# Optimization experiments

Hardware: AMD Instinct MI355X
Metric: run time of the kernel (lower is better)

Reference implementation:

```python
import jax, jax.numpy as jnp
import numpy as np


def _ln(x, g, b):
    mu = x.mean(-1, keepdims=True)
    var = ((x - mu) ** 2).mean(-1, keepdims=True)
    return (x - mu) * jax.lax.rsqrt(var + 1e-5) * g + b


def _gelu(x):
    return jax.nn.gelu(x, approximate=False)  # torch nn.GELU default (exact)


def setup_inputs() -> dict:
    key = jax.random.key(0)
    ks = iter(jax.random.split(key, 64))
    N, E, D, H, P, DT, FF, L = 30000, 480000, 128, 4, 5, 32, 512, 2
    w = lambda *s: 0.02 * jax.random.normal(next(ks), s, jnp.float32)
    return dict(
        triplet_h=jax.random.normal(next(ks), (N, D), jnp.float32),
        path_len_emb=w(P + 1, D), vp_emb=w(D), sl_emb=w(D),
        dW1=w(D, D), db1=jnp.zeros(D), dW2=w(D, H), db2=jnp.zeros(H),
        tWin=w(P, D, DT), tbin=jnp.zeros((P, DT)), tWout=w(P, DT, DT), tbout=jnp.zeros((P, DT)),
        pW1=w(DT, DT), pb1=jnp.zeros(DT), pW2=w(DT, H), pb2=jnp.zeros(H),
        ln1_g=jnp.ones((L, D)), ln1_b=jnp.zeros((L, D)),
        qkv_W=w(L, D, 3 * D), qkv_b=jnp.zeros((L, 3 * D)),
        res_ln_g=jnp.ones((L, D)), res_ln_b=jnp.zeros((L, D)),
        res_W=w(L, D, D), res_b=jnp.zeros((L, D)),
        ffn_Win=w(L, D, FF), ffn_bin=jnp.zeros((L, FF)),
        ffn_Wout=w(L, FF, D), ffn_bout=jnp.zeros((L, D)),
        src=jax.random.randint(next(ks), (E,), 0, N, jnp.int32),
        dst=jax.random.randint(next(ks), (E,), 0, N, jnp.int32),
        path=jax.random.randint(next(ks), (E, P), 0, N, jnp.int32),
        vp=jax.random.randint(next(ks), (E,), 0, 2, jnp.int32),
        sl=jax.random.randint(next(ks), (E,), 0, 2, jnp.int32),
    )


def reference(triplet_h, path_len_emb, vp_emb, sl_emb,
              dW1, db1, dW2, db2, tWin, tbin, tWout, tbout,
              pW1, pb1, pW2, pb2, ln1_g, ln1_b, qkv_W, qkv_b,
              res_ln_g, res_ln_b, res_W, res_b,
              ffn_Win, ffn_bin, ffn_Wout, ffn_bout,
              src, dst, path, vp, sl):
    N, D = triplet_h.shape
    H = dW2.shape[1]
    dh = D // H
    L = qkv_W.shape[0]
    P = path.shape[1]
    DT = tWout.shape[-1]
    scale = D ** (-0.5)

    # _featurize_path: path length embedding + virtual/self-loop overrides
    path = jnp.where(path < -99, -1, path)
    mask = path >= 0
    plen = mask.sum(-1)
    pf = path_len_emb[plen]                                   # [E, D]
    pf = jnp.where((vp == 1)[:, None], vp_emb[None, :], pf)
    pf = jnp.where((sl == 1)[:, None], sl_emb[None, :], pf)
    dist_attn = _gelu(pf @ dW1 + db1) @ dW2 + db2             # [E, H]

    # _init_path: per-position MLP on triplets, gather along paths, mean
    acc = jnp.zeros((path.shape[0], DT), triplet_h.dtype)
    for i in range(P):
        tab = _gelu(triplet_h @ tWin[i] + tbin[i]) @ tWout[i] + tbout[i]  # [N, DT]
        tab = jnp.concatenate([tab, jnp.zeros((1, DT), tab.dtype)], axis=0)
        idx = jnp.where(path[:, i] < 0, N, path[:, i])
        acc = acc + tab[idx]
    path_size = jnp.maximum(mask.sum(-1, keepdims=True), 1).astype(acc.dtype)
    path_h = acc / path_size                                  # [E, DT]
    path_attn = _gelu(path_h @ pW1 + pb1) @ pW2 + pb2         # [E, H]

    for l in range(L):
        h = _ln(triplet_h, ln1_g[l], ln1_b[l])
        qkv = (h @ qkv_W[l] + qkv_b[l]).reshape(N, 3, H, dh)
        q = qkv[:, 0] * scale
        k = qkv[:, 1]
        v = qkv[:, 2]
        # u_dot_v('Q','K'): Q lives on src, K on dst
        node_attn = jnp.einsum('ehd,ehd->eh', q[src], k[dst])  # [E, H]
        a = node_attn + dist_attn + path_attn
        # edge_softmax over incoming edges of each dst node
        m = jax.ops.segment_max(a, dst, num_segments=N)
        ex = jnp.exp(a - m[dst])
        s = jax.ops.segment_sum(ex, dst, num_segments=N)
        sa = ex / s[dst]                                       # [E, H]
        # message = src value weighted by attn, scatter-sum to dst
        he = (v[src] * sa[..., None]).reshape(-1, D)
        agg = jax.ops.segment_sum(he, dst, num_segments=N)     # [N, D]
        # Residual block
        x = triplet_h + agg @ res_W[l] + res_b[l]
        y = _ln(x, res_ln_g[l], res_ln_b[l])
        y = _gelu(y @ ffn_Win[l] + ffn_bin[l]) @ ffn_Wout[l] + ffn_bout[l]
        triplet_h = x + y
    return triplet_h
```

## Files before the change

kernel.cpp:

```cpp
#include <hip/hip_runtime.h>
#include <math.h>

#define D   128
#define H   4
#define PP  5
#define DT  32
#define FF  512
#define NL  2
#define SCALE 0.08838834764831845f

typedef _Float16 f16x8 __attribute__((ext_vector_type(8)));
typedef _Float16 f16x2 __attribute__((ext_vector_type(2)));
typedef float    f32x4 __attribute__((ext_vector_type(4)));

__device__ __forceinline__ float gelu(float x) {
    return 0.5f * x * (1.0f + erff(x * 0.7071067811865476f));
}

__device__ __forceinline__ f16x8 f16x8_zero() {
    f16x8 v;
#pragma unroll
    for (int j = 0; j < 8; ++j) v[j] = (_Float16)0.0f;
    return v;
}

#define NWP 18
struct WPrep {
    const float* src[NWP];
    _Float16*    dst[NWP];
    int K[NWP], C[NWP];
};

__global__ __launch_bounds__(256) void k_wprep(WPrep p) {
    int m = blockIdx.y;
    int n = blockIdx.x * 256 + threadIdx.x;
    int K = p.K[m], C = p.C[m];
    if (n >= K * C) return;
    int c = n / K, k = n - c * K;
    p.dst[m][n] = (_Float16)p.src[m][(size_t)k * C + c];
}

__global__ __launch_bounds__(256) void k_dist_tab(
    const float* __restrict__ ple, const float* __restrict__ vpe, const float* __restrict__ sle,
    const float* __restrict__ dW1, const float* __restrict__ db1,
    const float* __restrict__ dW2, const float* __restrict__ db2,
    float* __restrict__ dist_tab)
{
    __shared__ float pf[8][D];
    __shared__ float hid[8][D];
    int t = threadIdx.x;
    for (int i = t; i < 8 * D; i += 256) {
        int r = i >> 7, c = i & 127;
        float v;
        if (r < 6)      v = ple[r * D + c];
        else if (r == 6) v = vpe[c];
        else             v = sle[c];
        pf[r][c] = v;
    }
    __syncthreads();
    for (int i = t; i < 8 * D; i += 256) {
        int r = i >> 7, c = i & 127;
        float s = db1[c];
        for (int k = 0; k < D; ++k) s += pf[r][k] * dW1[k * D + c];
        hid[r][c] = gelu(s);
    }
    __syncthreads();
    if (t < 8 * H) {
        int r = t >> 2, h = t & 3;
        float s = db2[h];
        for (int k = 0; k < D; ++k) s += hid[r][k] * dW2[k * H + h];
        dist_tab[r * H + h] = s;
    }
}

__global__ __launch_bounds__(256) void k_tab_mfma(
    const float* __restrict__ X,
    const _Float16* __restrict__ Wt1,
    const float* __restrict__ tbin,
    const _Float16* __restrict__ Wt2,
    const float* __restrict__ tbout,
    float* __restrict__ tab, int N)
{
    __shared__ _Float16 Ah[64][136];
    __shared__ _Float16 hidS[4][16][40];
    int t = threadIdx.x;
    int n0 = blockIdx.x * 64;
#pragma unroll
    for (int i = 0; i < 4; ++i) {
        int flat = t + i * 256;
        int r = flat >> 4, c = flat & 15;
        f16x8 v = f16x8_zero();
        if (n0 + r < N) {
            const float* xp = X + (size_t)(n0 + r) * D + c * 8;
            float4 x0 = *(const float4*)xp;
            float4 x1 = *(const float4*)(xp + 4);
            v[0] = (_Float16)x0.x; v[1] = (_Float16)x0.y;
            v[2] = (_Float16)x0.z; v[3] = (_Float16)x0.w;
            v[4] = (_Float16)x1.x; v[5] = (_Float16)x1.y;
            v[6] = (_Float16)x1.z; v[7] = (_Float16)x1.w;
        }
        *(f16x8*)&Ah[r][c * 8] = v;
    }
    __syncthreads();
    int w = t >> 6, lane = t & 63;
    int rt0 = w * 16, lr = lane & 15, lg = lane >> 4;
    f16x8 a1[4];
#pragma unroll
    for (int kk = 0; kk < 4; ++kk)
        a1[kk] = *(const f16x8*)&Ah[rt0 + lr][kk * 32 + lg * 8];

    for (int i = 0; i < PP; ++i) {
#pragma unroll
        for (int ct = 0; ct < 2; ++ct) {
            int col = ct * 16 + lr;
            f32x4 c1 = {0.f, 0.f, 0.f, 0.f};
#pragma unroll
            for (int kk = 0; kk < 4; ++kk) {
                f16x8 b = *(const f16x8*)&Wt1[((size_t)i * DT + col) * 128 + kk * 32 + lg * 8];
                c1 = __builtin_amdgcn_mfma_f32_16x16x32_f16(a1[kk], b, c1, 0, 0, 0);
            }
            float bb = tbin[i * DT + col];
#pragma unroll
            for (int j = 0; j < 4; ++j)
                hidS[w][lg * 4 + j][col] = (_Float16)gelu(c1[j] + bb);
        }
        f16x8 a2 = *(const f16x8*)&hidS[w][lr][lg * 8];
#pragma unroll
        for (int ct = 0; ct < 2; ++ct) {
            int col = ct * 16 + lr;
            f32x4 c2 = {0.f, 0.f, 0.f, 0.f};
            f16x8 b2 = *(const f16x8*)&Wt2[((size_t)i * DT + col) * DT + lg * 8];
            c2 = __builtin_amdgcn_mfma_f32_16x16x32_f16(a2, b2, c2, 0, 0, 0);
            float bb = tbout[i * DT + col];
#pragma unroll
            for (int j = 0; j < 4; ++j) {
                int row = n0 + rt0 + lg * 4 + j;
                if (row < N) tab[((size_t)i * N + row) * DT + col] = c2[j] + bb;
            }
        }
    }
}

__global__ __launch_bounds__(256) void k_edge_pre(
    const int* __restrict__ path, const int* __restrict__ vp, const int* __restrict__ sl,
    const float* __restrict__ tab, const float* __restrict__ dist_tab,
    const float* __restrict__ pW1, const float* __restrict__ pb1,
    const float* __restrict__ pW2, const float* __restrict__ pb2,
    float* __restrict__ base_attn, int E, int N)
{
    __shared__ float W1t[DT][DT];
    __shared__ float W2s[DT][H];
    __shared__ float b1s[DT];
    __shared__ float b2s[H];
    __shared__ float dts[8][H];
    int t = threadIdx.x;
    for (int i = t; i < DT * DT; i += 256) {
        int k = i >> 5, c = i & 31;
        W1t[c][k] = pW1[i];
    }
    if (t < DT * H) W2s[t >> 2][t & 3] = pW2[t];
    if (t < DT) b1s[t] = pb1[t];
    if (t < H)  b2s[t] = pb2[t];
    if (t < 32) dts[t >> 2][t & 3] = dist_tab[t];
    __syncthreads();
    int e = blockIdx.x * 256 + t;
    if (e >= E) return;
    int pl = 0;
    float acc[DT];
#pragma unroll
    for (int c = 0; c < DT; ++c) acc[c] = 0.0f;
#pragma unroll
    for (int i = 0; i < PP; ++i) {
        int p = path[(size_t)e * PP + i];
        if (p < -99) p = -1;
        if (p >= 0) {
            ++pl;
            const float* row = tab + ((size_t)i * N + p) * DT;
#pragma unroll
            for (int c4 = 0; c4 < 8; ++c4) {
                float4 v = *(const float4*)(row + c4 * 4);
                acc[c4 * 4 + 0] += v.x; acc[c4 * 4 + 1] += v.y;
                acc[c4 * 4 + 2] += v.z; acc[c4 * 4 + 3] += v.w;
            }
        }
    }
    float inv = 1.0f / (float)(pl > 0 ? pl : 1);
#pragma unroll
    for (int c = 0; c < DT; ++c) acc[c] *= inv;
    float o0 = b2s[0], o1 = b2s[1], o2 = b2s[2], o3 = b2s[3];
    for (int c = 0; c < DT; ++c) {
        float s = b1s[c];
#pragma unroll
        for (int k4 = 0; k4 < 8; ++k4) {
            float4 w = *(const float4*)&W1t[c][k4 * 4];
            s += acc[k4 * 4 + 0] * w.x + acc[k4 * 4 + 1] * w.y +
                 acc[k4 * 4 + 2] * w.z + acc[k4 * 4 + 3] * w.w;
        }
        float hv = gelu(s);
        o0 += hv * W2s[c][0]; o1 += hv * W2s[c][1];
        o2 += hv * W2s[c][2]; o3 += hv * W2s[c][3];
    }
    int se = (sl[e] == 1) ? 7 : ((vp[e] == 1) ? 6 : pl);
    float4 ov = make_float4(o0 + dts[se][0], o1 + dts[se][1],
                            o2 + dts[se][2], o3 + dts[se][3]);
    *(float4*)(base_attn + (size_t)e * 4) = ov;
}

__global__ void k_count(const int* __restrict__ dst, int* __restrict__ deg, int E) {
    int e = blockIdx.x * 256 + threadIdx.x;
    if (e < E) atomicAdd(&deg[dst[e]], 1);
}

__global__ __launch_bounds__(1024) void k_scan(const int* __restrict__ deg,
                                               int* __restrict__ rowstart, int N) {
    __shared__ int sdata[1024];
    __shared__ int soff;
    int t = threadIdx.x;
    if (t == 0) soff = 0;
    for (int base = 0; base < N; base += 1024) {
        int v = (base + t < N) ? deg[base + t] : 0;
        __syncthreads();
        sdata[t] = v;
        __syncthreads();
        for (int off = 1; off < 1024; off <<= 1) {
            int x = (t >= off) ? sdata[t - off] : 0;
            __syncthreads();
            sdata[t] += x;
            __syncthreads();
        }
        int incl  = sdata[t];
        int total = sdata[1023];
        if (base + t < N) rowstart[base + t] = soff + incl - v;
        __syncthreads();
        if (t == 0) soff += total;
    }
    __syncthreads();
    if (t == 0) rowstart[N] = soff;
}

__global__ void k_scatter(const int* __restrict__ dst, const int* __restrict__ rowstart,
                          int* __restrict__ cursor, int* __restrict__ el, int E) {
    int e = blockIdx.x * 256 + threadIdx.x;
    if (e >= E) return;
    int d = dst[e];
    int pos = atomicAdd(&cursor[d], 1);
    el[rowstart[d] + pos] = e;
}

__global__ __launch_bounds__(256) void k_ln(const float* __restrict__ X, const float* __restrict__ g,
                                            const float* __restrict__ b, _Float16* __restrict__ out, int N) {
    int gw   = (blockIdx.x * 256 + threadIdx.x) >> 6;
    int lane = threadIdx.x & 63;
    if (gw >= N) return;
    const float* x = X + (size_t)gw * D;
    float a0 = x[lane], a1 = x[lane + 64];
    float s = a0 + a1;
#pragma unroll
    for (int m = 1; m < 64; m <<= 1) s += __shfl_xor(s, m);
    float mu = s * (1.0f / 128.0f);
    float d0 = a0 - mu, d1 = a1 - mu;
    float v = d0 * d0 + d1 * d1;
#pragma unroll
    for (int m = 1; m < 64; m <<= 1) v += __shfl_xor(v, m);
    float r = rsqrtf(v * (1.0f / 128.0f) + 1e-5f);
    _Float16* o = out + (size_t)gw * D;
    o[lane]      = (_Float16)(d0 * r * g[lane]      + b[lane]);
    o[lane + 64] = (_Float16)(d1 * r * g[lane + 64] + b[lane + 64]);
}


__global__ __launch_bounds__(256) void k_qkv_mfma(
    const _Float16* __restrict__ Hin, const _Float16* __restrict__ Wt,
    const float* __restrict__ bias, _Float16* __restrict__ C, int N)
{
    __shared__ _Float16 Ah[64][136];
    int t = threadIdx.x;
    int n0 = blockIdx.x * 64;
#pragma unroll
    for (int i = 0; i < 4; ++i) {
        int flat = t + i * 256;
        int r = flat >> 4, c = flat & 15;
        f16x8 v = f16x8_zero();
        if (n0 + r < N) v = *(const f16x8*)&Hin[(size_t)(n0 + r) * D + c * 8];
        *(f16x8*)&Ah[r][c * 8] = v;
    }
    __syncthreads();
    int w = t >> 6, lane = t & 63;
    int rt0 = w * 16, lr = lane & 15, lg = lane >> 4;
    f16x8 a1[4];
#pragma unroll
    for (int kk = 0; kk < 4; ++kk)
        a1[kk] = *(const f16x8*)&Ah[rt0 + lr][kk * 32 + lg * 8];
#pragma unroll 4
    for (int ct = 0; ct < 24; ++ct) {
        int col = ct * 16 + lr;
        f32x4 acc = {0.f, 0.f, 0.f, 0.f};
#pragma unroll
        for (int kk = 0; kk < 4; ++kk) {
            f16x8 b = *(const f16x8*)&Wt[(size_t)col * 128 + kk * 32 + lg * 8];
            acc = __builtin_amdgcn_mfma_f32_16x16x32_f16(a1[kk], b, acc, 0, 0, 0);
        }
        float bb = bias[col];
#pragma unroll
        for (int i = 0; i < 4; ++i) {
            int row = n0 + rt0 + lg * 4 + i;
            if (row < N) C[(size_t)row * 384 + col] = (_Float16)(acc[i] + bb);
        }
    }
}

__global__ __launch_bounds__(256) void k_res_mfma(
    const _Float16* __restrict__ Agg, const _Float16* __restrict__ Wt,
    const float* __restrict__ bias, const float* __restrict__ resid,
    float* __restrict__ Out, int N)
{
    __shared__ _Float16 Ah[64][136];
    int t = threadIdx.x;
    int n0 = blockIdx.x * 64;
#pragma unroll
    for (int i = 0; i < 4; ++i) {
        int flat = t + i * 256;
        int r = flat >> 4, c = flat & 15;
        f16x8 v = f16x8_zero();
        if (n0 + r < N) v = *(const f16x8*)&Agg[(size_t)(n0 + r) * D + c * 8];
        *(f16x8*)&Ah[r][c * 8] = v;
    }
    __syncthreads();
    int w = t >> 6, lane = t & 63;
    int rt0 = w * 16, lr = lane & 15, lg = lane >> 4;
    f16x8 a1[4];
#pragma unroll
    for (int kk = 0; kk < 4; ++kk)
        a1[kk] = *(const f16x8*)&Ah[rt0 + lr][kk * 32 + lg * 8];
#pragma unroll
    for (int ct = 0; ct < 8; ++ct) {
        int col = ct * 16 + lr;
        f32x4 acc = {0.f, 0.f, 0.f, 0.f};
#pragma unroll
        for (int kk = 0; kk < 4; ++kk) {
            f16x8 b = *(const f16x8*)&Wt[(size_t)col * 128 + kk * 32 + lg * 8];
            acc = __builtin_amdgcn_mfma_f32_16x16x32_f16(a1[kk], b, acc, 0, 0, 0);
        }
        float bb = bias[col];
#pragma unroll
        for (int i = 0; i < 4; ++i) {
            int row = n0 + rt0 + lg * 4 + i;
            if (row < N) {
                size_t o = (size_t)row * D + col;
                Out[o] = resid[o] + acc[i] + bb;
            }
        }
    }
}

__global__ __launch_bounds__(256) void k_ffn_mfma(
    const _Float16* __restrict__ Hin, const float* __restrict__ Xres,
    const _Float16* __restrict__ Wt1,
    const float* __restrict__ bin,
    const _Float16* __restrict__ Wt2,
    const float* __restrict__ bout,
    float* __restrict__ Out, int N)
{
    __shared__ _Float16 Ah[64][136];
    __shared__ _Float16 hid[64][264];
    int t = threadIdx.x;
    int n0 = blockIdx.x * 64;
#pragma unroll
    for (int i = 0; i < 4; ++i) {
        int flat = t + i * 256;
        int r = flat >> 4, c = flat & 15;
        f16x8 v = f16x8_zero();
        if (n0 + r < N) v = *(const f16x8*)&Hin[(size_t)(n0 + r) * D + c * 8];
        *(f16x8*)&Ah[r][c * 8] = v;
    }
    __syncthreads();
    int w = t >> 6, lane = t & 63;
    int rt0 = w * 16, lr = lane & 15, lg = lane >> 4;
    f16x8 a1[4];
#pragma unroll
    for (int kk = 0; kk < 4; ++kk)
        a1[kk] = *(const f16x8*)&Ah[rt0 + lr][kk * 32 + lg * 8];

    f32x4 acc2[8];
#pragma unroll
    for (int i = 0; i < 8; ++i) acc2[i] = (f32x4){0.f, 0.f, 0.f, 0.f};

    for (int ch = 0; ch < 2; ++ch) {
#pragma unroll 4
        for (int ct = 0; ct < 16; ++ct) {
            int hc = ch * 256 + ct * 16 + lr;
            f32x4 c1 = {0.f, 0.f, 0.f, 0.f};
#pragma unroll
            for (int kk = 0; kk < 4; ++kk) {
                f16x8 b = *(const f16x8*)&Wt1[(size_t)hc * 128 + kk * 32 + lg * 8];
                c1 = __builtin_amdgcn_mfma_f32_16x16x32_f16(a1[kk], b, c1, 0, 0, 0);
            }
            float bb = bin[hc];
#pragma unroll
            for (int i = 0; i < 4; ++i) {
                float v = gelu(c1[i] + bb);
                hid[rt0 + lg * 4 + i][ct * 16 + lr] = (_Float16)v;
            }
        }
#pragma unroll 2
        for (int kk2 = 0; kk2 < 8; ++kk2) {
            f16x8 a2 = *(const f16x8*)&hid[rt0 + lr][kk2 * 32 + lg * 8];
            int gk = ch * 256 + kk2 * 32 + lg * 8;
#pragma unroll
            for (int ct2 = 0; ct2 < 8; ++ct2) {
                f16x8 b2 = *(const f16x8*)&Wt2[(size_t)(ct2 * 16 + lr) * 512 + gk];
                acc2[ct2] = __builtin_amdgcn_mfma_f32_16x16x32_f16(a2, b2, acc2[ct2], 0, 0, 0);
            }
        }
    }
#pragma unroll
    for (int ct2 = 0; ct2 < 8; ++ct2) {
        int col = ct2 * 16 + lr;
        float bb = bout[col];
#pragma unroll
        for (int i = 0; i < 4; ++i) {
            int row = n0 + rt0 + lg * 4 + i;
            if (row < N) {
                size_t o = (size_t)row * D + col;
                Out[o] = Xres[o] + acc2[ct2][i] + bb;
            }
        }
    }
}

__global__ __launch_bounds__(256) void k_attn_agg(
    const _Float16* __restrict__ qkv,
    const int* __restrict__ rowstart, const int* __restrict__ el,
    const int* __restrict__ src, const float* __restrict__ base_attn,
    _Float16* __restrict__ agg, int N)
{
    int gw   = (blockIdx.x * 256 + threadIdx.x) >> 6;
    int lane = threadIdx.x & 63;
    if (gw >= N) return;
    int head = lane >> 4;
    f16x2 kk = *(const f16x2*)&qkv[(size_t)gw * 384 + 128 + 2 * lane];
    float k0 = (float)kk[0], k1 = (float)kk[1];
    int beg = rowstart[gw], end = rowstart[gw + 1];
    float s = 0.0f, a0 = 0.0f, a1 = 0.0f;
    int i = beg;
    for (; i + 4 <= end; i += 4) {
        int   e[4], sr[4];
        f16x2 qq[4], vv[4];
        float bb[4], tt[4];
#pragma unroll
        for (int j = 0; j < 4; ++j) e[j] = el[i + j];
#pragma unroll
        for (int j = 0; j < 4; ++j) sr[j] = src[e[j]];
#pragma unroll
        for (int j = 0; j < 4; ++j) {
            const _Float16* row = qkv + (size_t)sr[j] * 384;
            qq[j] = *(const f16x2*)&row[2 * lane];
            vv[j] = *(const f16x2*)&row[256 + 2 * lane];
            bb[j] = base_attn[(size_t)e[j] * 4 + head];
        }
#pragma unroll
        for (int j = 0; j < 4; ++j)
            tt[j] = (float)qq[j][0] * k0 + (float)qq[j][1] * k1;
#pragma unroll
        for (int m = 1; m <= 8; m <<= 1) {
#pragma unroll
            for (int j = 0; j < 4; ++j) tt[j] += __shfl_xor(tt[j], m);
        }
#pragma unroll
        for (int j = 0; j < 4; ++j) {
            float ex = expf(tt[j] * SCALE + bb[j]);
            s  += ex;
            a0 += ex * (float)vv[j][0];
            a1 += ex * (float)vv[j][1];
        }
    }
    for (; i < end; ++i) {
        int e  = el[i];
        int sr = src[e];
        const _Float16* row = qkv + (size_t)sr * 384;
        f16x2 qq = *(const f16x2*)&row[2 * lane];
        float t = (float)qq[0] * k0 + (float)qq[1] * k1;
#pragma unroll
        for (int m = 1; m <= 8; m <<= 1) t += __shfl_xor(t, m);
        float ex = expf(t * SCALE + base_attn[(size_t)e * 4 + head]);
        f16x2 vv = *(const f16x2*)&row[256 + 2 * lane];
        s  += ex;
        a0 += ex * (float)vv[0];
        a1 += ex * (float)vv[1];
    }
    float inv = (s > 0.0f) ? 1.0f / s : 0.0f;
    f16x2 o;
    o[0] = (_Float16)(a0 * inv);
    o[1] = (_Float16)(a1 * inv);
    *(f16x2*)&agg[(size_t)gw * D + 2 * lane] = o;
}

extern "C" void kernel_launch(void* const* d_in, const int* in_sizes, int n_in,
                              void* d_out, int out_size, void* d_ws, size_t ws_size,
                              hipStream_t stream) {
    const float* triplet_h = (const float*)d_in[0];
    const float* ple    = (const float*)d_in[1];
    const float* vpe    = (const float*)d_in[2];
    const float* sle    = (const float*)d_in[3];
    const float* dW1    = (const float*)d_in[4];
    const float* db1    = (const float*)d_in[5];
    const float* dW2    = (const float*)d_in[6];
    const float* db2    = (const float*)d_in[7];
    const float* tWin   = (const float*)d_in[8];
    const float* tbin   = (const float*)d_in[9];
    const float* tWout  = (const float*)d_in[10];
    const float* tbout  = (const float*)d_in[11];
    const float* pW1    = (const float*)d_in[12];
    const float* pb1    = (const float*)d_in[13];
    const float* pW2    = (const float*)d_in[14];
    const float* pb2    = (const float*)d_in[15];
    const float* ln1_g  = (const float*)d_in[16];
    const float* ln1_b  = (const float*)d_in[17];
    const float* qkv_W  = (const float*)d_in[18];
    const float* qkv_b  = (const float*)d_in[19];
    const float* rln_g  = (const float*)d_in[20];
    const float* rln_b  = (const float*)d_in[21];
    const float* res_W  = (const float*)d_in[22];
    const float* res_b  = (const float*)d_in[23];
    const float* fWin   = (const float*)d_in[24];
    const float* fbin   = (const float*)d_in[25];
    const float* fWout  = (const float*)d_in[26];
    const float* fbout  = (const float*)d_in[27];
    const int*   srcp   = (const int*)d_in[28];
    const int*   dstp   = (const int*)d_in[29];
    const int*   path   = (const int*)d_in[30];
    const int*   vp     = (const int*)d_in[31];
    const int*   sl     = (const int*)d_in[32];

    const int N = in_sizes[0] / D;
    const int E = in_sizes[28];

    char* ws = (char*)d_ws;
    size_t off = 0;
    auto alloc = [&](size_t bytes) -> void* {
        void* p = ws + off;
        off += (bytes + 255) & ~(size_t)255;
        return p;
    };
    float*     tab      = (float*)alloc((size_t)PP * N * DT * 4);
    float*     dist_tab = (float*)alloc(8 * H * 4);
    float*     base_attn= (float*)alloc((size_t)E * H * 4);
    int*       deg      = (int*)alloc((size_t)N * 4);
    int*       rowstart = (int*)alloc((size_t)(N + 1) * 4);
    int*       cursor   = (int*)alloc((size_t)N * 4);
    int*       el       = (int*)alloc((size_t)E * 4);
    _Float16*  hbuf     = (_Float16*)alloc((size_t)N * D * 2);
    _Float16*  qkvbuf   = (_Float16*)alloc((size_t)N * 384 * 2);
    _Float16*  aggbuf   = (_Float16*)alloc((size_t)N * D * 2);
    float*     bufA     = (float*)alloc((size_t)N * D * 4);
    float*     bufB     = (float*)alloc((size_t)N * D * 4);
    _Float16*  WtQ      = (_Float16*)alloc((size_t)NL * 384 * 128 * 2);
    _Float16*  WtR      = (_Float16*)alloc((size_t)NL * 128 * 128 * 2);
    _Float16*  Wt1      = (_Float16*)alloc((size_t)NL * 512 * 128 * 2);
    _Float16*  Wt2      = (_Float16*)alloc((size_t)NL * 128 * 512 * 2);
    _Float16*  WtTin    = (_Float16*)alloc((size_t)PP * DT * 128 * 2);
    _Float16*  WtTout   = (_Float16*)alloc((size_t)PP * DT * DT * 2);
    if (off > ws_size) return;

    hipMemsetAsync(deg,    0, (size_t)N * 4, stream);
    hipMemsetAsync(cursor, 0, (size_t)N * 4, stream);

    WPrep wp;
    wp.src[0] = qkv_W;                wp.dst[0] = WtQ;               wp.K[0] = 128; wp.C[0] = 384;
    wp.src[1] = qkv_W + 128 * 384;    wp.dst[1] = WtQ + 384 * 128;   wp.K[1] = 128; wp.C[1] = 384;
    wp.src[2] = res_W;                wp.dst[2] = WtR;               wp.K[2] = 128; wp.C[2] = 128;
    wp.src[3] = res_W + 128 * 128;    wp.dst[3] = WtR + 128 * 128;   wp.K[3] = 128; wp.C[3] = 128;
    wp.src[4] = fWin;                 wp.dst[4] = Wt1;               wp.K[4] = 128; wp.C[4] = 512;
    wp.src[5] = fWin + 128 * 512;     wp.dst[5] = Wt1 + 512 * 128;   wp.K[5] = 128; wp.C[5] = 512;
    wp.src[6] = fWout;                wp.dst[6] = Wt2;               wp.K[6] = 512; wp.C[6] = 128;
    wp.src[7] = fWout + 512 * 128;    wp.dst[7] = Wt2 + 128 * 512;   wp.K[7] = 512; wp.C[7] = 128;
    for (int i = 0; i < PP; ++i) {
        wp.src[8 + i]  = tWin  + (size_t)i * 128 * DT;
        wp.dst[8 + i]  = WtTin + (size_t)i * DT * 128;
        wp.K[8 + i] = 128; wp.C[8 + i] = DT;
        wp.src[13 + i] = tWout  + (size_t)i * DT * DT;
        wp.dst[13 + i] = WtTout + (size_t)i * DT * DT;
        wp.K[13 + i] = DT; wp.C[13 + i] = DT;
    }
    k_wprep<<<dim3(256, NWP), 256, 0, stream>>>(wp);

    k_dist_tab<<<1, 256, 0, stream>>>(ple, vpe, sle, dW1, db1, dW2, db2, dist_tab);
    k_tab_mfma<<<(N + 63) / 64, 256, 0, stream>>>(triplet_h, WtTin, tbin, WtTout, tbout, tab, N);
    k_edge_pre<<<(E + 255) / 256, 256, 0, stream>>>(path, vp, sl, tab, dist_tab,
                                                    pW1, pb1, pW2, pb2, base_attn, E, N);
    k_count<<<(E + 255) / 256, 256, 0, stream>>>(dstp, deg, E);
    k_scan<<<1, 1024, 0, stream>>>(deg, rowstart, N);
    k_scatter<<<(E + 255) / 256, 256, 0, stream>>>(dstp, rowstart, cursor, el, E);

    hipMemcpyAsync(bufA, triplet_h, (size_t)N * D * 4, hipMemcpyDeviceToDevice, stream);

    for (int l = 0; l < NL; ++l) {
        k_ln<<<(N + 3) / 4, 256, 0, stream>>>(bufA, ln1_g + l * D, ln1_b + l * D, hbuf, N);
        k_qkv_mfma<<<(N + 63) / 64, 256, 0, stream>>>(hbuf, WtQ + (size_t)l * 384 * 128,
                                                      qkv_b + l * 384, qkvbuf, N);
        k_attn_agg<<<(N + 3) / 4, 256, 0, stream>>>(qkvbuf, rowstart, el, srcp,
                                                    base_attn, aggbuf, N);
        k_res_mfma<<<(N + 63) / 64, 256, 0, stream>>>(aggbuf, WtR + (size_t)l * 128 * 128,
                                                      res_b + l * D, bufA, bufB, N);
        k_ln<<<(N + 3) / 4, 256, 0, stream>>>(bufB, rln_g + l * D, rln_b + l * D, hbuf, N);
        k_ffn_mfma<<<(N + 63) / 64, 256, 0, stream>>>(hbuf, bufB,
                                                      Wt1 + (size_t)l * 512 * 128, fbin + l * FF,
                                                      Wt2 + (size_t)l * 128 * 512, fbout + l * D,
                                                      bufA, N);
    }

    hipMemcpyAsync(d_out, bufA, (size_t)N * D * 4, hipMemcpyDeviceToDevice, stream);
}
```

Before: 710.0 us.

## Split QKV and FFN MFMA work by output columns across waves instead of rows

In the QKV and FFN kernels, each wave now keeps all 64 rows of A in registers and handles a disjoint slice of output columns. Before, each wave took 16 rows and loaded every weight column. Each weight fragment is now loaded once per block rather than once per wave, cutting global/L2 weight traffic by four. The FFN hidden tile is now shared across waves, so barriers are added around its use, and register pressure from the larger A and accumulator arrays goes up.

```diff
diff --git a/kernel.cpp b/kernel.cpp
--- a/kernel.cpp
+++ b/kernel.cpp
@@ -286,25 +286,32 @@
     }
     __syncthreads();
     int w = t >> 6, lane = t & 63;
-    int rt0 = w * 16, lr = lane & 15, lg = lane >> 4;
-    f16x8 a1[4];
-#pragma unroll
-    for (int kk = 0; kk < 4; ++kk)
-        a1[kk] = *(const f16x8*)&Ah[rt0 + lr][kk * 32 + lg * 8];
-#pragma unroll 4
-    for (int ct = 0; ct < 24; ++ct) {
-        int col = ct * 16 + lr;
-        f32x4 acc = {0.f, 0.f, 0.f, 0.f};
-#pragma unroll
-        for (int kk = 0; kk < 4; ++kk) {
-            f16x8 b = *(const f16x8*)&Wt[(size_t)col * 128 + kk * 32 + lg * 8];
-            acc = __builtin_amdgcn_mfma_f32_16x16x32_f16(a1[kk], b, acc, 0, 0, 0);
-        }
+    int lr = lane & 15, lg = lane >> 4;
+    f16x8 a1[4][4];
+#pragma unroll
+    for (int rt = 0; rt < 4; ++rt)
+#pragma unroll
+        for (int kk = 0; kk < 4; ++kk)
+            a1[rt][kk] = *(const f16x8*)&Ah[rt * 16 + lr][kk * 32 + lg * 8];
+#pragma unroll 2
+    for (int ct = 0; ct < 6; ++ct) {
+        int col = w * 96 + ct * 16 + lr;
+        f16x8 b[4];
+#pragma unroll
+        for (int kk = 0; kk < 4; ++kk)
+            b[kk] = *(const f16x8*)&Wt[(size_t)col * 128 + kk * 32 + lg * 8];
         float bb = bias[col];
 #pragma unroll
-        for (int i = 0; i < 4; ++i) {
-            int row = n0 + rt0 + lg * 4 + i;
-            if (row < N) C[(size_t)row * 384 + col] = (_Float16)(acc[i] + bb);
+        for (int rt = 0; rt < 4; ++rt) {
+            f32x4 acc = {0.f, 0.f, 0.f, 0.f};
+#pragma unroll
+            for (int kk = 0; kk < 4; ++kk)
+                acc = __builtin_amdgcn_mfma_f32_16x16x32_f16(a1[rt][kk], b[kk], acc, 0, 0, 0);
+#pragma unroll
+            for (int i = 0; i < 4; ++i) {
+                int row = n0 + rt * 16 + lg * 4 + i;
+                if (row < N) C[(size_t)row * 384 + col] = (_Float16)(acc[i] + bb);
+            }
         }
     }
 }
@@ -375,56 +382,72 @@
     }
     __syncthreads();
     int w = t >> 6, lane = t & 63;
-    int rt0 = w * 16, lr = lane & 15, lg = lane >> 4;
-    f16x8 a1[4];
-#pragma unroll
-    for (int kk = 0; kk < 4; ++kk)
-        a1[kk] = *(const f16x8*)&Ah[rt0 + lr][kk * 32 + lg * 8];
-
-    f32x4 acc2[8];
-#pragma unroll
-    for (int i = 0; i < 8; ++i) acc2[i] = (f32x4){0.f, 0.f, 0.f, 0.f};
+    int lr = lane & 15, lg = lane >> 4;
+    f16x8 a1[4][4];
+#pragma unroll
+    for (int rt = 0; rt < 4; ++rt)
+#pragma unroll
+        for (int kk = 0; kk < 4; ++kk)
+            a1[rt][kk] = *(const f16x8*)&Ah[rt * 16 + lr][kk * 32 + lg * 8];
+
+    f32x4 acc2[2][4];
+#pragma unroll
+    for (int c = 0; c < 2; ++c)
+#pragma unroll
+        for (int r = 0; r < 4; ++r) acc2[c][r] = (f32x4){0.f, 0.f, 0.f, 0.f};
 
     for (int ch = 0; ch < 2; ++ch) {
-#pragma unroll 4
-        for (int ct = 0; ct < 16; ++ct) {
-            int hc = ch * 256 + ct * 16 + lr;
-            f32x4 c1 = {0.f, 0.f, 0.f, 0.f};
-#pragma unroll
-            for (int kk = 0; kk < 4; ++kk) {
-                f16x8 b = *(const f16x8*)&Wt1[(size_t)hc * 128 + kk * 32 + lg * 8];
-                c1 = __builtin_amdgcn_mfma_f32_16x16x32_f16(a1[kk], b, c1, 0, 0, 0);
-            }
-            float bb = bin[hc];
-#pragma unroll
-            for (int i = 0; i < 4; ++i) {
-                float v = gelu(c1[i] + bb);
-                hid[rt0 + lg * 4 + i][ct * 16 + lr] = (_Float16)v;
-            }
-        }
+#pragma unroll
+        for (int ct = 0; ct < 4; ++ct) {
+            int colg = ch * 256 + w * 64 + ct * 16 + lr;
+            f16x8 b[4];
+#pragma unroll
+            for (int kk = 0; kk < 4; ++kk)
+                b[kk] = *(const f16x8*)&Wt1[(size_t)colg * 128 + kk * 32 + lg * 8];
+            float bb = bin[colg];
+#pragma unroll
+            for (int rt = 0; rt < 4; ++rt) {
+                f32x4 c1 = {0.f, 0.f, 0.f, 0.f};
+#pragma unroll
+                for (int kk = 0; kk < 4; ++kk)
+                    c1 = __builtin_amdgcn_mfma_f32_16x16x32_f16(a1[rt][kk], b[kk], c1, 0, 0, 0);
+#pragma unroll
+                for (int j = 0; j < 4; ++j)
+                    hid[rt * 16 + lg * 4 + j][w * 64 + ct * 16 + lr] = (_Float16)gelu(c1[j] + bb);
+            }
+        }
+        __syncthreads();
 #pragma unroll 2
         for (int kk2 = 0; kk2 < 8; ++kk2) {
-            f16x8 a2 = *(const f16x8*)&hid[rt0 + lr][kk2 * 32 + lg * 8];
-            int gk = ch * 256 + kk2 * 32 + lg * 8;
-#pragma unroll
-            for (int ct2 = 0; ct2 < 8; ++ct2) {
-                f16x8 b2 = *(const f16x8*)&Wt2[(size_t)(ct2 * 16 + lr) * 512 + gk];
-                acc2[ct2] = __builtin_amdgcn_mfma_f32_16x16x32_f16(a2, b2, acc2[ct2], 0, 0, 0);
-            }
-        }
-    }
-#pragma unroll
-    for (int ct2 = 0; ct2 < 8; ++ct2) {
-        int col = ct2 * 16 + lr;
-        float bb = bout[col];
-#pragma unroll
-        for (int i = 0; i < 4; ++i) {
-            int row = n0 + rt0 + lg * 4 + i;
-            if (row < N) {
-                size_t o = (size_t)row * D + col;
-                Out[o] = Xres[o] + acc2[ct2][i] + bb;
-            }
-        }
+            f16x8 a2[4];
+#pragma unroll
+            for (int rt = 0; rt < 4; ++rt)
+                a2[rt] = *(const f16x8*)&hid[rt * 16 + lr][kk2 * 32 + lg * 8];
+#pragma unroll
+            for (int ct2 = 0; ct2 < 2; ++ct2) {
+                int colo = w * 32 + ct2 * 16 + lr;
+                f16x8 b2 = *(const f16x8*)&Wt2[(size_t)colo * 512 + ch * 256 + kk2 * 32 + lg * 8];
+#pragma unroll
+                for (int rt = 0; rt < 4; ++rt)
+                    acc2[ct2][rt] = __builtin_amdgcn_mfma_f32_16x16x32_f16(a2[rt], b2, acc2[ct2][rt], 0, 0, 0);
+            }
+        }
+        __syncthreads();
+    }
+#pragma unroll
+    for (int ct2 = 0; ct2 < 2; ++ct2) {
+        int colo = w * 32 + ct2 * 16 + lr;
+        float bb = bout[colo];
+#pragma unroll
+        for (int rt = 0; rt < 4; ++rt)
+#pragma unroll
+            for (int i = 0; i < 4; ++i) {
+                int row = n0 + rt * 16 + lg * 4 + i;
+                if (row < N) {
+                    size_t o = (size_t)row * D + colo;
+                    Out[o] = Xres[o] + acc2[ct2][rt][i] + bb;
+                }
+            }
     }
 }
 
```

Result: faster. 615.0 us (-13.4%).
